# Optimization experiments

Hardware: AMD Instinct MI355X
Metric: run time of the kernel (lower is better)

## Reference

```python
import jax, jax.numpy as jnp
import numpy as np

N_STEPS = 32
DELTA = 1.0 / N_STEPS
LOG_2PI = float(np.log(2.0 * np.pi))


def _v_field(a, s, t_col, W1, b1, W2, b2, W3, b3):
    # SharedVNet: MLP([a_t, s, t]) -> (v_c, r); role='expert' => v = v_c + r
    x = jnp.concatenate([a, s, t_col], axis=-1)          # [B, a_dim+s_dim+1]
    h = jax.nn.relu(x @ W1 + b1)                          # [B, 128]
    h = jax.nn.relu(h @ W2 + b2)                          # [B, 128]
    out = h @ W3 + b3                                     # [B, 2*a_dim]
    v_c, r = jnp.split(out, 2, axis=-1)
    return v_c + r


def setup_inputs() -> dict:
    key = jax.random.key(0)
    ks = jax.random.split(key, 8)
    B, S, A, H = 65536, 64, 16, 128
    IN = A + S + 1
    s = jax.random.normal(ks[0], (B, S), dtype=jnp.float32)
    a0 = jax.random.normal(ks[1], (B, A), dtype=jnp.float32)
    rad = jax.random.randint(ks[2], (N_STEPS, B, A), 0, 2).astype(jnp.int32)
    W1 = jax.random.normal(ks[3], (IN, H), dtype=jnp.float32) / np.sqrt(IN)
    b1 = jnp.zeros((H,), dtype=jnp.float32)
    W2 = jax.random.normal(ks[4], (H, H), dtype=jnp.float32) / np.sqrt(H)
    b2 = jnp.zeros((H,), dtype=jnp.float32)
    W3 = jax.random.normal(ks[5], (H, 2 * A), dtype=jnp.float32) / np.sqrt(H)
    b3 = jnp.zeros((2 * A,), dtype=jnp.float32)
    return {"s": s, "a0": a0, "rad": rad, "W1": W1, "b1": b1,
            "W2": W2, "b2": b2, "W3": W3, "b3": b3}


def reference(s, a0, rad, W1, b1, W2, b2, W3, b3):
    B, a_dim = a0.shape
    t_grid = jnp.linspace(0.0, 1.0, N_STEPS + 1)
    t_mids = 0.5 * (t_grid[:-1] + t_grid[1:])             # [32]
    rad_f = 2.0 * rad.astype(jnp.float32) - 1.0           # Rademacher +/-1
    ones_col = jnp.ones((B, 1), dtype=a0.dtype)

    def step(carry, xs):
        a_t, log_det = carry
        t_mid, v = xs
        a_t = jax.lax.stop_gradient(a_t)                  # a_t.detach().requires_grad_(True)
        t_col = t_mid * ones_col
        f = lambda a: _v_field(a, s, t_col, W1, b1, W2, b2, W3, b3)
        v_t, vjp_fn = jax.vjp(f, a_t)
        jv, = vjp_fn(v)                                   # v^T J  (Hutchinson)
        div = jnp.sum(jv * v, axis=-1)                    # [B]
        log_det = log_det - DELTA * div
        a_t = a_t + jax.lax.stop_gradient(v_t) * DELTA    # v_t.detach() Euler update
        return (a_t, log_det), None

    init = (a0, jnp.zeros((B,), dtype=a0.dtype))
    (a_T, log_det), _ = jax.lax.scan(step, init, (t_mids, rad_f))
    # standard Normal(0,1) log_prob summed over action dims
    logp_prior = jnp.sum(-0.5 * a_T * a_T - 0.5 * LOG_2PI, axis=-1)
    return logp_prior + log_det
```

## Files before the change

kernel.cpp:

```cpp
#include <hip/hip_runtime.h>
#include <hip/hip_bf16.h>
#include <stdint.h>

#define NSTEP   32
#define BATCH   65536
#define NTHR    512
#define RPB     256
#define DELTA_F (1.0f/32.0f)
#define LN2PI_F 1.83787706640934534f

#define RB1 208
#define RB2 304
#define RB3 272
#define OFF_W1 0
#define OFF_W2 26624
#define OFF_W3 65536
#define LDS_BYTES 74240

typedef __attribute__((ext_vector_type(8)))  short    s16x8;
typedef __attribute__((ext_vector_type(8)))  __bf16   bf16x8;
typedef __attribute__((ext_vector_type(4)))  float    f32x4;
typedef __attribute__((ext_vector_type(16))) float    f32x16;
typedef __attribute__((ext_vector_type(4)))  int      i32x4;
typedef __attribute__((ext_vector_type(4)))  unsigned u32x4;

#define Z16 ((f32x16){0,0,0,0,0,0,0,0,0,0,0,0,0,0,0,0})

static __device__ __forceinline__ f32x16 mfma32(s16x8 a, s16x8 b, f32x16 c){
    return __builtin_amdgcn_mfma_f32_32x32x16_bf16(
        __builtin_bit_cast(bf16x8, a), __builtin_bit_cast(bf16x8, b), c, 0, 0, 0);
}

static __device__ __forceinline__ unsigned short f2bf(float f){
    union { float f; unsigned u; } v; v.f = f;
    unsigned u = v.u + 0x7fffu + ((v.u >> 16) & 1u);
    return (unsigned short)(u >> 16);
}

static __device__ __forceinline__ float bf2f(unsigned short b){
    return __uint_as_float(((unsigned)b) << 16);
}

static __device__ __forceinline__ unsigned cvtpk(float lo, float hi){
    unsigned r;
    asm("v_cvt_pk_bf16_f32 %0, %1, %2" : "=v"(r) : "v"(lo), "v"(hi));
    return r;
}

static __device__ __forceinline__ void pswap(unsigned &a, unsigned &b){
    auto r = __builtin_amdgcn_permlane32_swap((int)a, (int)b, false, false);
    a = (unsigned)r[0]; b = (unsigned)r[1];
}

static __device__ __forceinline__ s16x8 pconv(i32x4 u0, i32x4 u1){
    const unsigned P = 0x3F80u, M = 0xBF80u;
    u32x4 d;
    d[0] = (u0[0] ? P : M) | ((u0[1] ? P : M) << 16);
    d[1] = (u0[2] ? P : M) | ((u0[3] ? P : M) << 16);
    d[2] = (u1[0] ? P : M) | ((u1[1] ? P : M) << 16);
    d[3] = (u1[2] ? P : M) | ((u1[3] ? P : M) << 16);
    return __builtin_bit_cast(s16x8, d);
}

static __device__ __forceinline__ void pack_tr(const f32x16 h, const f32x16 tt,
        s16x8* bA, s16x8* bB, s16x8* tA, s16x8* tB){
    unsigned Ph[8], Pt[8];
#pragma unroll
    for (int q = 0; q < 8; ++q){
        float h0 = h[2*q], h1 = h[2*q+1];
        float r0 = h0 > 0.f ? h0 : 0.f,      r1 = h1 > 0.f ? h1 : 0.f;
        float s0 = h0 > 0.f ? tt[2*q] : 0.f, s1 = h1 > 0.f ? tt[2*q+1] : 0.f;
        Ph[q] = cvtpk(r0, r1);
        Pt[q] = cvtpk(s0, s1);
    }
    pswap(Ph[0], Ph[2]); pswap(Ph[1], Ph[3]); pswap(Ph[4], Ph[6]); pswap(Ph[5], Ph[7]);
    pswap(Pt[0], Pt[2]); pswap(Pt[1], Pt[3]); pswap(Pt[4], Pt[6]); pswap(Pt[5], Pt[7]);
    *bA = __builtin_bit_cast(s16x8, (u32x4){Ph[0], Ph[1], Ph[2], Ph[3]});
    *bB = __builtin_bit_cast(s16x8, (u32x4){Ph[4], Ph[5], Ph[6], Ph[7]});
    *tA = __builtin_bit_cast(s16x8, (u32x4){Pt[0], Pt[1], Pt[2], Pt[3]});
    *tB = __builtin_bit_cast(s16x8, (u32x4){Pt[4], Pt[5], Pt[6], Pt[7]});
}

__global__ __launch_bounds__(NTHR, 2)
void cfm_kernel(const float* __restrict__ s_g,
                const float* __restrict__ a0_g,
                const int*   __restrict__ rad_g,
                const float* __restrict__ W1g, const float* __restrict__ b1g,
                const float* __restrict__ W2g, const float* __restrict__ b2g,
                const float* __restrict__ W3g, const float* __restrict__ b3g,
                float* __restrict__ out_g)
{
    extern __shared__ char lds[];
    const int tid  = threadIdx.x;
    const int lane = tid & 63;
    const int wv   = tid >> 6;
    const int c32  = lane & 31;
    const int hi   = lane >> 5;

    unsigned short* W1t = (unsigned short*)(lds + OFF_W1);
    unsigned short* W2t = (unsigned short*)(lds + OFF_W2);
    unsigned short* W3c = (unsigned short*)(lds + OFF_W3);

    for (int idx = tid; idx < 128*104; idx += NTHR){
        int n = idx / 104, k = idx % 104;
        float v = 0.f;
        if (k < 80)       v = W1g[k*128 + n];
        else if (k == 80) v = b1g[n];
        else if (k == 81) v = W1g[80*128 + n];
        else if (k == 82){ float w = W1g[80*128 + n]; v = w - bf2f(f2bf(w)); }
        else if (k == 83){ float bb = b1g[n];         v = bb - bf2f(f2bf(bb)); }
        W1t[n*104 + k] = f2bf(v);
    }
    for (int idx = tid; idx < 128*152; idx += NTHR){
        int n = idx / 152, k = idx % 152;
        float v = 0.f;
        if (k < 128)       v = W2g[k*128 + n];
        else if (k == 128) v = b2g[n];
        else if (k == 129){ float bb = b2g[n]; v = bb - bf2f(f2bf(bb)); }
        W2t[n*152 + k] = f2bf(v);
    }
    for (int idx = tid; idx < 32*136; idx += NTHR){
        int m = idx / 136, k = idx % 136;
        float v = (m < 16 && k < 128) ? (W3g[k*32 + m] + W3g[k*32 + 16 + m]) : 0.f;
        W3c[m*136 + k] = f2bf(v);
    }
    __syncthreads();

    const char* pW1 = lds + OFF_W1 + c32*RB1 + hi*16;
    const char* pW2 = lds + OFF_W2 + c32*RB2 + hi*16;
    const char* pW3 = lds + OFF_W3 + c32*RB3 + hi*16;

    const int row = blockIdx.x * RPB + wv*32 + c32;

    const float* srow = s_g + (size_t)row * 64;
    s16x8 xk1, xk2, xk3, xk4;
    {
        auto mk_s = [&](int K)->s16x8{
            f32x4 u = *(const f32x4*)(srow + 16*(K-1) + 8*hi);
            f32x4 w = *(const f32x4*)(srow + 16*(K-1) + 8*hi + 4);
            return __builtin_bit_cast(s16x8, (u32x4){
                cvtpk(u[0],u[1]), cvtpk(u[2],u[3]), cvtpk(w[0],w[1]), cvtpk(w[2],w[3])});
        };
        xk1 = mk_s(1); xk2 = mk_s(2); xk3 = mk_s(3); xk4 = mk_s(4);
    }

    f32x4 av0 = *(const f32x4*)(a0_g + (size_t)row*16 + 4*hi);
    f32x4 av1 = *(const f32x4*)(a0_g + (size_t)row*16 + 8 + 4*hi);

    auto mk_a = [&]()->s16x8{
        unsigned A0 = cvtpk(av0[0],av0[1]), A1 = cvtpk(av0[2],av0[3]);
        unsigned B0 = cvtpk(av1[0],av1[1]), B1 = cvtpk(av1[2],av1[3]);
        pswap(A0, B0); pswap(A1, B1);
        return __builtin_bit_cast(s16x8, (u32x4){A0, A1, B0, B1});
    };
    s16x8 xk0 = mk_a();

    f32x4 b3c0, b3c1;
    {
        f32x4 p0 = *(const f32x4*)(b3g + 4*hi);
        f32x4 p1 = *(const f32x4*)(b3g + 16 + 4*hi);
        f32x4 p2 = *(const f32x4*)(b3g + 8 + 4*hi);
        f32x4 p3 = *(const f32x4*)(b3g + 24 + 4*hi);
        b3c0 = p0 + p1; b3c1 = p2 + p3;
    }

    const int* rp = rad_g + ((size_t)row << 4);
    s16x8 pf;
    {
        i32x4 a = *(const i32x4*)(rp + 8*hi);
        i32x4 b = *(const i32x4*)(rp + 8*hi + 4);
        pf = pconv(a, b);
    }

    float ldet = 0.0f;

    for (int t = 0; t < NSTEP; ++t){
        const float tmid = ((float)t + 0.5f) * DELTA_F;
        const int* rpN = rp + (size_t)BATCH*16;

        i32x4 pn0 = {0,0,0,0}, pn1 = {0,0,0,0};
        if (t + 1 < NSTEP){
            pn0 = *(const i32x4*)(rpN + 8*hi);
            pn1 = *(const i32x4*)(rpN + 8*hi + 4);
        }
        i32x4 us0 = *(const i32x4*)(rp + 4*hi);
        i32x4 us1 = *(const i32x4*)(rp + 8 + 4*hi);

        s16x8 xk5;
        {
            unsigned tb = (unsigned)f2bf(tmid);
            unsigned s0 = hi ? 0u : (0x3F80u | (tb << 16));
            unsigned s1 = hi ? 0u : (tb | (0x3F80u << 16));
            xk5 = __builtin_bit_cast(s16x8, (u32x4){s0, s1, 0u, 0u});
        }

        f32x16 F[4], T[4];
        {
            unsigned b8 = hi ? 0u : 0x3F803F80u;
            s16x8 bb = __builtin_bit_cast(s16x8, (u32x4){b8, 0u, 0u, 0u});
#pragma unroll
            for (int Mo = 0; Mo < 4; ++Mo){
                s16x8 w28 = *(const s16x8*)(pW2 + Mo*9728 + 8*32);
                F[Mo] = mfma32(w28, bb, Z16);
                T[Mo] = Z16;
            }
        }

        __builtin_amdgcn_s_setprio(1);
#pragma unroll
        for (int M = 0; M < 4; ++M){
            s16x8 w10 = *(const s16x8*)(pW1 + M*6656);
            f32x16 h  = mfma32(w10, xk0, Z16);
            f32x16 tt = mfma32(w10, pf,  Z16);
            h = mfma32(*(const s16x8*)(pW1 + M*6656 +  32), xk1, h);
            h = mfma32(*(const s16x8*)(pW1 + M*6656 +  64), xk2, h);
            h = mfma32(*(const s16x8*)(pW1 + M*6656 +  96), xk3, h);
            h = mfma32(*(const s16x8*)(pW1 + M*6656 + 128), xk4, h);
            h = mfma32(*(const s16x8*)(pW1 + M*6656 + 160), xk5, h);

            s16x8 bhA, bhB, btA, btB;
            pack_tr(h, tt, &bhA, &bhB, &btA, &btB);
#pragma unroll
            for (int Mo = 0; Mo < 4; ++Mo){
                s16x8 w2a = *(const s16x8*)(pW2 + Mo*9728 + (2*M)*32);
                F[Mo] = mfma32(w2a, bhA, F[Mo]);
                T[Mo] = mfma32(w2a, btA, T[Mo]);
                s16x8 w2b = *(const s16x8*)(pW2 + Mo*9728 + (2*M+1)*32);
                F[Mo] = mfma32(w2b, bhB, F[Mo]);
                T[Mo] = mfma32(w2b, btB, T[Mo]);
            }
        }

        f32x16 vf = {b3c0[0], b3c0[1], b3c0[2], b3c0[3],
                     b3c1[0], b3c1[1], b3c1[2], b3c1[3],
                     0,0,0,0,0,0,0,0};
        f32x16 vt = Z16;
#pragma unroll
        for (int M = 0; M < 4; ++M){
            s16x8 qhA, qhB, qtA, qtB;
            pack_tr(F[M], T[M], &qhA, &qhB, &qtA, &qtB);
            s16x8 w3a = *(const s16x8*)(pW3 + (2*M)*32);
            vf = mfma32(w3a, qhA, vf);
            vt = mfma32(w3a, qtA, vt);
            s16x8 w3b = *(const s16x8*)(pW3 + (2*M+1)*32);
            vf = mfma32(w3b, qhB, vf);
            vt = mfma32(w3b, qtB, vt);
        }
        __builtin_amdgcn_s_setprio(0);

        av0[0] += DELTA_F * vf[0]; av0[1] += DELTA_F * vf[1];
        av0[2] += DELTA_F * vf[2]; av0[3] += DELTA_F * vf[3];
        av1[0] += DELTA_F * vf[4]; av1[1] += DELTA_F * vf[5];
        av1[2] += DELTA_F * vf[6]; av1[3] += DELTA_F * vf[7];
        xk0 = mk_a();

        {
            int g0 = us0[0] ? 0 : (int)0x80000000u;
            int g1 = us0[1] ? 0 : (int)0x80000000u;
            int g2 = us0[2] ? 0 : (int)0x80000000u;
            int g3 = us0[3] ? 0 : (int)0x80000000u;
            int g4 = us1[0] ? 0 : (int)0x80000000u;
            int g5 = us1[1] ? 0 : (int)0x80000000u;
            int g6 = us1[2] ? 0 : (int)0x80000000u;
            int g7 = us1[3] ? 0 : (int)0x80000000u;
            float q0 = __int_as_float(__float_as_int(vf[0]*0.f + vt[0]) ^ g0);
            float q1 = __int_as_float(__float_as_int(vt[1]) ^ g1);
            float q2 = __int_as_float(__float_as_int(vt[2]) ^ g2);
            float q3 = __int_as_float(__float_as_int(vt[3]) ^ g3);
            float q4 = __int_as_float(__float_as_int(vt[4]) ^ g4);
            float q5 = __int_as_float(__float_as_int(vt[5]) ^ g5);
            float q6 = __int_as_float(__float_as_int(vt[6]) ^ g6);
            float q7 = __int_as_float(__float_as_int(vt[7]) ^ g7);
            float prod = ((q0 + q1) + (q2 + q3)) + ((q4 + q5) + (q6 + q7));
            unsigned pu = __float_as_uint(prod), pv = pu;
            pswap(pu, pv);
            prod = __uint_as_float(pu) + __uint_as_float(pv);
            ldet -= DELTA_F * prod;
        }

        pf = pconv(pn0, pn1);
        rp = rpN;
    }

    float asq = av0[0]*av0[0] + av0[1]*av0[1] + av0[2]*av0[2] + av0[3]*av0[3]
              + av1[0]*av1[0] + av1[1]*av1[1] + av1[2]*av1[2] + av1[3]*av1[3];
    {
        unsigned pu = __float_as_uint(asq), pv = pu;
        pswap(pu, pv);
        asq = __uint_as_float(pu) + __uint_as_float(pv);
    }
    if (hi == 0)
        out_g[row] = -0.5f*asq - 8.0f*LN2PI_F + ldet;
}

extern "C" void kernel_launch(void* const* d_in, const int* in_sizes, int n_in,
                              void* d_out, int out_size, void* d_ws, size_t ws_size,
                              hipStream_t stream)
{
    const float* s_g  = (const float*)d_in[0];
    const float* a0_g = (const float*)d_in[1];
    const int*   rad  = (const int*)  d_in[2];
    const float* W1   = (const float*)d_in[3];
    const float* b1   = (const float*)d_in[4];
    const float* W2   = (const float*)d_in[5];
    const float* b2   = (const float*)d_in[6];
    const float* W3   = (const float*)d_in[7];
    const float* b3   = (const float*)d_in[8];
    float* out = (float*)d_out;

    hipFuncSetAttribute(reinterpret_cast<const void*>(cfm_kernel),
                        hipFuncAttributeMaxDynamicSharedMemorySize, LDS_BYTES);

    cfm_kernel<<<BATCH/RPB, NTHR, LDS_BYTES, stream>>>(
        s_g, a0_g, rad, W1, b1, W2, b2, W3, b3, out);
}
```

Baseline: 215.5 us.

## Stagger wave start, reorder MFMA chains and software-pipeline layer-3 packing

Half of the waves in each block sleep briefly after weight staging, so the waves fall out of phase and contend less for the MFMA unit. The xk0 MFMA, which depends on the previous step's action, moves to the end of the layer-1 chain so the state-independent products can start first. setprio is narrowed to the layer-2 and layer-3 MFMA bursts, and the layer-3 pack_tr is double-buffered to overlap with the MFMAs. The prefetch branch becomes an unconditional load with a clamped offset, the loop is unrolled by two, and a leftover vf*0 dependency is removed. The trade-offs are an initial idle delay and higher register pressure from the unrolling.

```diff
diff --git a/kernel.cpp b/kernel.cpp
--- a/kernel.cpp
+++ b/kernel.cpp
@@ -126,6 +126,8 @@
     }
     __syncthreads();
 
+    if (wv >= 4) __builtin_amdgcn_s_sleep(63);
+
     const char* pW1 = lds + OFF_W1 + c32*RB1 + hi*16;
     const char* pW2 = lds + OFF_W2 + c32*RB2 + hi*16;
     const char* pW3 = lds + OFF_W3 + c32*RB3 + hi*16;
@@ -174,15 +176,14 @@
 
     float ldet = 0.0f;
 
+#pragma unroll 2
     for (int t = 0; t < NSTEP; ++t){
         const float tmid = ((float)t + 0.5f) * DELTA_F;
-        const int* rpN = rp + (size_t)BATCH*16;
-
-        i32x4 pn0 = {0,0,0,0}, pn1 = {0,0,0,0};
-        if (t + 1 < NSTEP){
-            pn0 = *(const i32x4*)(rpN + 8*hi);
-            pn1 = *(const i32x4*)(rpN + 8*hi + 4);
-        }
+        const size_t adv = (t + 1 < NSTEP) ? (size_t)BATCH*16 : (size_t)0;
+        const int* rpS = rp + adv;
+
+        i32x4 pn0 = *(const i32x4*)(rpS + 8*hi);
+        i32x4 pn1 = *(const i32x4*)(rpS + 8*hi + 4);
         i32x4 us0 = *(const i32x4*)(rp + 4*hi);
         i32x4 us1 = *(const i32x4*)(rp + 8 + 4*hi);
 
@@ -206,20 +207,20 @@
             }
         }
 
-        __builtin_amdgcn_s_setprio(1);
 #pragma unroll
         for (int M = 0; M < 4; ++M){
             s16x8 w10 = *(const s16x8*)(pW1 + M*6656);
-            f32x16 h  = mfma32(w10, xk0, Z16);
-            f32x16 tt = mfma32(w10, pf,  Z16);
-            h = mfma32(*(const s16x8*)(pW1 + M*6656 +  32), xk1, h);
+            f32x16 tt = mfma32(w10, pf, Z16);
+            f32x16 h  = mfma32(*(const s16x8*)(pW1 + M*6656 +  32), xk1, Z16);
             h = mfma32(*(const s16x8*)(pW1 + M*6656 +  64), xk2, h);
             h = mfma32(*(const s16x8*)(pW1 + M*6656 +  96), xk3, h);
             h = mfma32(*(const s16x8*)(pW1 + M*6656 + 128), xk4, h);
             h = mfma32(*(const s16x8*)(pW1 + M*6656 + 160), xk5, h);
+            h = mfma32(w10, xk0, h);
 
             s16x8 bhA, bhB, btA, btB;
             pack_tr(h, tt, &bhA, &bhB, &btA, &btB);
+            __builtin_amdgcn_s_setprio(1);
 #pragma unroll
             for (int Mo = 0; Mo < 4; ++Mo){
                 s16x8 w2a = *(const s16x8*)(pW2 + Mo*9728 + (2*M)*32);
@@ -229,24 +230,40 @@
                 F[Mo] = mfma32(w2b, bhB, F[Mo]);
                 T[Mo] = mfma32(w2b, btB, T[Mo]);
             }
+            __builtin_amdgcn_s_setprio(0);
         }
 
         f32x16 vf = {b3c0[0], b3c0[1], b3c0[2], b3c0[3],
                      b3c1[0], b3c1[1], b3c1[2], b3c1[3],
                      0,0,0,0,0,0,0,0};
         f32x16 vt = Z16;
-#pragma unroll
-        for (int M = 0; M < 4; ++M){
+        {
             s16x8 qhA, qhB, qtA, qtB;
-            pack_tr(F[M], T[M], &qhA, &qhB, &qtA, &qtB);
-            s16x8 w3a = *(const s16x8*)(pW3 + (2*M)*32);
-            vf = mfma32(w3a, qhA, vf);
-            vt = mfma32(w3a, qtA, vt);
-            s16x8 w3b = *(const s16x8*)(pW3 + (2*M+1)*32);
-            vf = mfma32(w3b, qhB, vf);
-            vt = mfma32(w3b, qtB, vt);
-        }
-        __builtin_amdgcn_s_setprio(0);
+            pack_tr(F[0], T[0], &qhA, &qhB, &qtA, &qtB);
+            __builtin_amdgcn_s_setprio(1);
+#pragma unroll
+            for (int M = 0; M < 4; ++M){
+                if (M < 3){
+                    s16x8 nhA, nhB, ntA, ntB;
+                    pack_tr(F[M+1], T[M+1], &nhA, &nhB, &ntA, &ntB);
+                    s16x8 w3a = *(const s16x8*)(pW3 + (2*M)*32);
+                    vf = mfma32(w3a, qhA, vf);
+                    vt = mfma32(w3a, qtA, vt);
+                    s16x8 w3b = *(const s16x8*)(pW3 + (2*M+1)*32);
+                    vf = mfma32(w3b, qhB, vf);
+                    vt = mfma32(w3b, qtB, vt);
+                    qhA = nhA; qhB = nhB; qtA = ntA; qtB = ntB;
+                } else {
+                    s16x8 w3a = *(const s16x8*)(pW3 + (2*M)*32);
+                    vf = mfma32(w3a, qhA, vf);
+                    vt = mfma32(w3a, qtA, vt);
+                    s16x8 w3b = *(const s16x8*)(pW3 + (2*M+1)*32);
+                    vf = mfma32(w3b, qhB, vf);
+                    vt = mfma32(w3b, qtB, vt);
+                }
+            }
+            __builtin_amdgcn_s_setprio(0);
+        }
 
         av0[0] += DELTA_F * vf[0]; av0[1] += DELTA_F * vf[1];
         av0[2] += DELTA_F * vf[2]; av0[3] += DELTA_F * vf[3];
@@ -263,7 +280,7 @@
             int g5 = us1[1] ? 0 : (int)0x80000000u;
             int g6 = us1[2] ? 0 : (int)0x80000000u;
             int g7 = us1[3] ? 0 : (int)0x80000000u;
-            float q0 = __int_as_float(__float_as_int(vf[0]*0.f + vt[0]) ^ g0);
+            float q0 = __int_as_float(__float_as_int(vt[0]) ^ g0);
             float q1 = __int_as_float(__float_as_int(vt[1]) ^ g1);
             float q2 = __int_as_float(__float_as_int(vt[2]) ^ g2);
             float q3 = __int_as_float(__float_as_int(vt[3]) ^ g3);
@@ -279,7 +296,7 @@
         }
 
         pf = pconv(pn0, pn1);
-        rp = rpN;
+        rp = rpS;
     }
 
     float asq = av0[0]*av0[0] + av0[1]*av0[1] + av0[2]*av0[2] + av0[3]*av0[3]
```

Measured after the change: 223.4 us. 3.7% more time.
